# Optimization experiments

Hardware: AMD Instinct MI355X
Metric: run time of the kernel (lower is better)

Reference implementation:

```python
import jax, jax.numpy as jnp
import numpy as np

T, B, I, H = 1024, 64, 512, 512


def setup_inputs() -> dict:
    key = jax.random.key(0)
    ks = jax.random.split(key, 16)
    s = 0.05  # weight init scale
    inp = {
        "x": jax.random.normal(ks[0], (T, B, I), jnp.float32),
        "h0": jax.random.normal(ks[1], (B, H), jnp.float32),
        "c0": jax.random.normal(ks[2], (B, H), jnp.float32),
        "W_ih0f": jax.random.normal(ks[3], (4 * H, I), jnp.float32) * s,
        "W_hh0f": jax.random.normal(ks[4], (4 * H, H), jnp.float32) * s,
        "b0f": jax.random.normal(ks[5], (4 * H,), jnp.float32) * s,
        "W_ih0b": jax.random.normal(ks[6], (4 * H, I), jnp.float32) * s,
        "W_hh0b": jax.random.normal(ks[7], (4 * H, H), jnp.float32) * s,
        "b0b": jax.random.normal(ks[8], (4 * H,), jnp.float32) * s,
        "W_ih1f": jax.random.normal(ks[9], (4 * H, 2 * H), jnp.float32) * s,
        "W_hh1f": jax.random.normal(ks[10], (4 * H, H), jnp.float32) * s,
        "b1f": jax.random.normal(ks[11], (4 * H,), jnp.float32) * s,
        "W_ih1b": jax.random.normal(ks[12], (4 * H, 2 * H), jnp.float32) * s,
        "W_hh1b": jax.random.normal(ks[13], (4 * H, H), jnp.float32) * s,
        "b1b": jax.random.normal(ks[14], (4 * H,), jnp.float32) * s,
    }
    return inp


def _lstm_dir(x, h0, c0, W_ih, W_hh, b, reverse):
    # x: [T, B, in]; precompute input contribution once (big GEMM)
    xg = jnp.einsum('tbi,gi->tbg', x, W_ih) + b  # [T, B, 4H]

    def step(carry, xt):
        h, c = carry
        g = xt + h @ W_hh.T  # [B, 4H]
        i, f, gg, o = jnp.split(g, 4, axis=-1)  # PyTorch LSTMCell gate order
        i = jax.nn.sigmoid(i)
        f = jax.nn.sigmoid(f)
        gg = jnp.tanh(gg)
        o = jax.nn.sigmoid(o)
        c2 = f * c + i * gg
        h2 = o * jnp.tanh(c2)
        return (h2, c2), h2

    (hT, cT), out = jax.lax.scan(step, (h0, c0), xg, reverse=reverse)
    return out, hT, cT  # out[t] aligned with input time t


def reference(x, h0, c0,
              W_ih0f, W_hh0f, b0f, W_ih0b, W_hh0b, b0b,
              W_ih1f, W_hh1f, b1f, W_ih1b, W_hh1b, b1b):
    layers = [
        ((W_ih0f, W_hh0f, b0f), (W_ih0b, W_hh0b, b0b)),
        ((W_ih1f, W_hh1f, b1f), (W_ih1b, W_hh1b, b1b)),
    ]
    inputs = x
    hn, cn = [], []
    for (fw, bw) in layers:
        # NOTE: original reuses the same init_hidden for every layer/direction
        out_f, hf, cf = _lstm_dir(inputs, h0, c0, *fw, reverse=False)
        out_b, hb, cb = _lstm_dir(inputs, h0, c0, *bw, reverse=True)
        hn.append(jnp.concatenate([hf, hb], axis=1))
        cn.append(jnp.concatenate([cf, cb], axis=1))
        inputs = jnp.concatenate([out_f, out_b], axis=2)  # [T, B, 2H]
    hn = jnp.stack(hn, axis=0)  # [L, B, 2H]
    cn = jnp.stack(cn, axis=0)
    return inputs, hn, cn
```

## Files before the change

kernel.cpp:

```cpp
#include <hip/hip_runtime.h>


using bfrag = __attribute__((ext_vector_type(8))) short;
using facc  = __attribute__((ext_vector_type(4))) float;

#define TT 1024
#define NB 64

#define FENCE_PRE(v)  asm volatile("s_nop 3" : "+v"(v))
#define FENCE_POST(v) asm volatile("s_nop 7\n\ts_nop 7" : "+v"(v))

__device__ __forceinline__ unsigned short f2bf(float f) {
  union { float f; unsigned u; } v; v.f = f;
  unsigned r = v.u + 0x7fffu + ((v.u >> 16) & 1u);
  return (unsigned short)(r >> 16);
}
__device__ __forceinline__ float sigm(float x)  { return 1.f / (1.f + __expf(-x)); }
__device__ __forceinline__ float tanhf_(float x){ return 1.f - 2.f / (__expf(2.f * x) + 1.f); }

__device__ __forceinline__ facc mfma_bf16(bfrag a, bfrag b, facc c) {
  asm("v_mfma_f32_16x16x32_bf16 %0, %1, %2, %0" : "+v"(c) : "v"(a), "v"(b));
  return c;
}

__global__ __launch_bounds__(256) void k_cvt_x(const float* __restrict__ x,
                                               unsigned short* __restrict__ xb) {
  int i = blockIdx.x * 256 + threadIdx.x;
  float4 v = reinterpret_cast<const float4*>(x)[i];
  ushort4 o;
  o.x = f2bf(v.x); o.y = f2bf(v.y); o.z = f2bf(v.z); o.w = f2bf(v.w);
  reinterpret_cast<ushort4*>(xb)[i] = o;
}

__global__ __launch_bounds__(256) void k_init(const float* __restrict__ h0,
                                              const float* __restrict__ c0,
                                              unsigned short* __restrict__ h0b,
                                              float* __restrict__ C4) {
  int i = blockIdx.x * 256 + threadIdx.x;
  h0b[i] = f2bf(h0[i]);
  float c = c0[i];
  C4[i] = c; C4[32768 + i] = c; C4[65536 + i] = c; C4[98304 + i] = c;
}

template <int KX>
__global__ __launch_bounds__(256) void k_pack(const float* __restrict__ Wih,
                                              const float* __restrict__ Whh,
                                              const float* __restrict__ bias,
                                              unsigned short* __restrict__ PW,
                                              float* __restrict__ PB) {
  constexpr int K = KX + 512;
  int tid = blockIdx.x * 256 + threadIdx.x;
  int R = tid / K;
  int k = tid - R * K;
  int g = R >> 4, r = R & 15;
  int q = r >> 2, gate = r & 3;
  int srow = gate * 512 + (g * 4 + q);
  float v = (k < KX) ? Wih[srow * KX + k] : Whh[srow * 512 + (k - KX)];
  PW[tid] = f2bf(v);
  if (k == 0) PB[R] = bias[srow];
}

template <int LAYER>
__global__ __launch_bounds__(256) void k_step(
    int s,
    const unsigned short* __restrict__ xin,
    unsigned short* __restrict__ y0,
    float* __restrict__ dout,
    const unsigned short* __restrict__ h0b,
    float* __restrict__ C4,
    unsigned short* __restrict__ hb,
    const unsigned short* __restrict__ PWf, const unsigned short* __restrict__ PWb,
    const float* __restrict__ PBf, const float* __restrict__ PBb) {
  constexpr int KX = (LAYER == 0) ? 512 : 1024;
  constexpr int K  = KX + 512;

  const int bid  = blockIdx.x;
  const int dir  = bid >> 7;
  const int hg   = bid & 127;
  const int t    = dir ? (TT - 1 - s) : s;
  const int wave = threadIdx.x >> 6;
  const int lane = threadIdx.x & 63;
  const int lr   = lane & 15;
  const int lq   = lane >> 4;
  const int b    = wave * 16 + lr;
  const bool first = (s == 0);
  const int tprev  = dir ? (t + 1) : (t - 1);

  const unsigned short* pw = dir ? PWb : PWf;
  const float* pb          = dir ? PBb : PBf;
  const unsigned short* Abase = pw + (size_t)(hg * 16 + lr) * K + lq * 8;

  const unsigned short* xrow = xin + ((size_t)t * NB + b) * (size_t)KX + lq * 8;

  const unsigned short* hrow;
  if (first)            hrow = h0b + (size_t)b * 512 + lq * 8;
  else if (LAYER == 0)  hrow = y0 + ((size_t)tprev * NB + b) * 1024 + dir * 512 + lq * 8;
  else                  hrow = hb + (size_t)((((s & 1) ^ 1) * 2 + dir)) * 32768 + (size_t)b * 512 + lq * 8;

  facc acc = {0.f, 0.f, 0.f, 0.f};
  FENCE_PRE(acc);

#pragma unroll 8
  for (int kk = 0; kk < KX / 32; ++kk) {
    bfrag a = *reinterpret_cast<const bfrag*>(Abase + kk * 32);
    bfrag x = *reinterpret_cast<const bfrag*>(xrow + kk * 32);
    acc = mfma_bf16(a, x, acc);
  }
#pragma unroll 8
  for (int kk = 0; kk < 16; ++kk) {
    bfrag a = *reinterpret_cast<const bfrag*>(Abase + KX + kk * 32);
    bfrag h = *reinterpret_cast<const bfrag*>(hrow + kk * 32);
    acc = mfma_bf16(a, h, acc);
  }
  FENCE_POST(acc);

  const int hcol = hg * 4 + lq;
  const int scan = LAYER * 2 + dir;
  float4 bias = *reinterpret_cast<const float4*>(pb + hg * 16 + lq * 4);
  float ig = sigm(acc[0] + bias.x);
  float fg = sigm(acc[1] + bias.y);
  float gv = tanhf_(acc[2] + bias.z);
  float og = sigm(acc[3] + bias.w);
  const int cidx = scan * 32768 + b * 512 + hcol;
  float c2 = fg * C4[cidx] + ig * gv;
  float h2 = og * tanhf_(c2);
  C4[cidx] = c2;

  const size_t orow = ((size_t)t * NB + b) * 1024 + dir * 512 + hcol;
  if (LAYER == 0) {
    y0[orow] = f2bf(h2);
  } else {
    dout[orow] = h2;
    hb[(size_t)((s & 1) * 2 + dir) * 32768 + (size_t)b * 512 + hcol] = f2bf(h2);
  }

  if (s == TT - 1) {
    const size_t oh = ((size_t)LAYER * NB + b) * 1024 + dir * 512 + hcol;
    dout[67108864 + oh] = h2;
    dout[67239936 + oh] = c2;
  }
}

extern "C" void kernel_launch(void* const* d_in, const int* in_sizes, int n_in,
                              void* d_out, int out_size, void* d_ws, size_t ws_size,
                              hipStream_t stream) {
  (void)in_sizes; (void)n_in; (void)out_size; (void)ws_size;
  const float* x  = (const float*)d_in[0];
  const float* h0 = (const float*)d_in[1];
  const float* c0 = (const float*)d_in[2];
  const float* W[12];
  for (int i = 0; i < 12; ++i) W[i] = (const float*)d_in[3 + i];

  char* ws = (char*)d_ws;
  unsigned short* xb   = (unsigned short*)(ws + 0ull);
  unsigned short* y0   = (unsigned short*)(ws + 67108864ull);
  unsigned short* h0b  = (unsigned short*)(ws + 201326592ull);
  unsigned short* PW0F = (unsigned short*)(ws + 201392128ull);
  unsigned short* PW0B = (unsigned short*)(ws + 205586432ull);
  unsigned short* PW1F = (unsigned short*)(ws + 209780736ull);
  unsigned short* PW1B = (unsigned short*)(ws + 216072192ull);
  float*          PB   = (float*)(ws + 222363648ull);
  float*          C4   = (float*)(ws + 222396416ull);
  unsigned short* hb   = (unsigned short*)(ws + 222920704ull);
  float* dout = (float*)d_out;

  k_cvt_x<<<32768, 256, 0, stream>>>(x, xb);
  k_init<<<128, 256, 0, stream>>>(h0, c0, h0b, C4);
  k_pack<512> <<<8192, 256, 0, stream>>>(W[0], W[1],  W[2],  PW0F, PB + 0);
  k_pack<512> <<<8192, 256, 0, stream>>>(W[3], W[4],  W[5],  PW0B, PB + 2048);
  k_pack<1024><<<12288, 256, 0, stream>>>(W[6], W[7],  W[8],  PW1F, PB + 4096);
  k_pack<1024><<<12288, 256, 0, stream>>>(W[9], W[10], W[11], PW1B, PB + 6144);

  for (int s = 0; s < TT; ++s)
    k_step<0><<<256, 256, 0, stream>>>(s, xb, y0, dout, h0b, C4, hb, PW0F, PW0B, PB + 0,    PB + 2048);
  for (int s = 0; s < TT; ++s)
    k_step<1><<<256, 256, 0, stream>>>(s, y0, y0, dout, h0b, C4, hb, PW1F, PW1B, PB + 4096, PB + 6144);
}
```

Measured before the change: 25.58 ms.

## Split LSTM into chunked input GEMM and persistent cooperative recurrent scan

Replaces the per-timestep kernel launches with two phases per 64-step chunk. First, a batched kernel precomputes the input-gate projection plus bias into a bf16 buffer. Then a persistent cooperative kernel keeps the recurrent weights in registers, stages h in LDS, and syncs its 16 blocks across timesteps with atomic flag polling. This removes about 2048 launch overheads and repeated weight reloads. In exchange, 16 blocks use very little of the GPU, inter-block spin-waits sit on the critical path, and rounding the precomputed gates to bf16 adds error.

Measured after the change: 38.15 ms. 1.49x slower.

```diff
diff --git a/kernel.cpp b/kernel.cpp
--- a/kernel.cpp
+++ b/kernel.cpp
@@ -3,24 +3,38 @@
 
 using bfrag = __attribute__((ext_vector_type(8))) short;
 using facc  = __attribute__((ext_vector_type(4))) float;
-
-#define TT 1024
-#define NB 64
-
-#define FENCE_PRE(v)  asm volatile("s_nop 3" : "+v"(v))
-#define FENCE_POST(v) asm volatile("s_nop 7\n\ts_nop 7" : "+v"(v))
+typedef unsigned long long u64;
 
 __device__ __forceinline__ unsigned short f2bf(float f) {
   union { float f; unsigned u; } v; v.f = f;
   unsigned r = v.u + 0x7fffu + ((v.u >> 16) & 1u);
   return (unsigned short)(r >> 16);
 }
+__device__ __forceinline__ float bf2f(unsigned short u) {
+  union { unsigned u; float f; } v; v.u = ((unsigned)u) << 16; return v.f;
+}
 __device__ __forceinline__ float sigm(float x)  { return 1.f / (1.f + __expf(-x)); }
 __device__ __forceinline__ float tanhf_(float x){ return 1.f - 2.f / (__expf(2.f * x) + 1.f); }
 
 __device__ __forceinline__ facc mfma_bf16(bfrag a, bfrag b, facc c) {
   asm("v_mfma_f32_16x16x32_bf16 %0, %1, %2, %0" : "+v"(c) : "v"(a), "v"(b));
   return c;
+}
+__device__ __forceinline__ u64 pack4bf(facc a) {
+  return (u64)f2bf(a[0]) | ((u64)f2bf(a[1]) << 16)
+       | ((u64)f2bf(a[2]) << 32) | ((u64)f2bf(a[3]) << 48);
+}
+__device__ __forceinline__ u64 ald(const u64* p) {
+  return __hip_atomic_load(p, __ATOMIC_RELAXED, __HIP_MEMORY_SCOPE_AGENT);
+}
+__device__ __forceinline__ unsigned ald32(const unsigned* p) {
+  return __hip_atomic_load(p, __ATOMIC_RELAXED, __HIP_MEMORY_SCOPE_AGENT);
+}
+__device__ __forceinline__ void ast16(unsigned short* p, unsigned short v) {
+  __hip_atomic_store(p, v, __ATOMIC_RELAXED, __HIP_MEMORY_SCOPE_AGENT);
+}
+__device__ __forceinline__ void ast32(unsigned* p, unsigned v) {
+  __hip_atomic_store(p, v, __ATOMIC_RELAXED, __HIP_MEMORY_SCOPE_AGENT);
 }
 
 __global__ __launch_bounds__(256) void k_cvt_x(const float* __restrict__ x,
@@ -35,11 +49,13 @@
 __global__ __launch_bounds__(256) void k_init(const float* __restrict__ h0,
                                               const float* __restrict__ c0,
                                               unsigned short* __restrict__ h0b,
-                                              float* __restrict__ C4) {
+                                              float* __restrict__ cbuf,
+                                              unsigned* __restrict__ hxf) {
   int i = blockIdx.x * 256 + threadIdx.x;
   h0b[i] = f2bf(h0[i]);
   float c = c0[i];
-  C4[i] = c; C4[32768 + i] = c; C4[65536 + i] = c; C4[98304 + i] = c;
+  cbuf[i] = c; cbuf[32768 + i] = c; cbuf[65536 + i] = c; cbuf[98304 + i] = c;
+  if (i < 128) hxf[i] = 0;
 }
 
 template <int KX>
@@ -61,84 +77,180 @@
 }
 
 template <int LAYER>
-__global__ __launch_bounds__(256) void k_step(
-    int s,
+__global__ __launch_bounds__(256) void k_xg(
+    int ph,
     const unsigned short* __restrict__ xin,
-    unsigned short* __restrict__ y0,
-    float* __restrict__ dout,
-    const unsigned short* __restrict__ h0b,
-    float* __restrict__ C4,
-    unsigned short* __restrict__ hb,
+    unsigned short* __restrict__ xgq,
     const unsigned short* __restrict__ PWf, const unsigned short* __restrict__ PWb,
     const float* __restrict__ PBf, const float* __restrict__ PBb) {
   constexpr int KX = (LAYER == 0) ? 512 : 1024;
   constexpr int K  = KX + 512;
-
-  const int bid  = blockIdx.x;
-  const int dir  = bid >> 7;
-  const int hg   = bid & 127;
-  const int t    = dir ? (TT - 1 - s) : s;
-  const int wave = threadIdx.x >> 6;
-  const int lane = threadIdx.x & 63;
-  const int lr   = lane & 15;
-  const int lq   = lane >> 4;
-  const int b    = wave * 16 + lr;
-  const bool first = (s == 0);
-  const int tprev  = dir ? (t + 1) : (t - 1);
-
+  const int bid = blockIdx.x;
+  const int dir = bid >> 7, hg = bid & 127;
+  const int wv = threadIdx.x >> 6, lane = threadIdx.x & 63;
+  const int lr = lane & 15, lq = lane >> 4;
+  const int b = wv * 16 + lr;
   const unsigned short* pw = dir ? PWb : PWf;
   const float* pb          = dir ? PBb : PBf;
   const unsigned short* Abase = pw + (size_t)(hg * 16 + lr) * K + lq * 8;
-
-  const unsigned short* xrow = xin + ((size_t)t * NB + b) * (size_t)KX + lq * 8;
-
-  const unsigned short* hrow;
-  if (first)            hrow = h0b + (size_t)b * 512 + lq * 8;
-  else if (LAYER == 0)  hrow = y0 + ((size_t)tprev * NB + b) * 1024 + dir * 512 + lq * 8;
-  else                  hrow = hb + (size_t)((((s & 1) ^ 1) * 2 + dir)) * 32768 + (size_t)b * 512 + lq * 8;
-
-  facc acc = {0.f, 0.f, 0.f, 0.f};
-  FENCE_PRE(acc);
-
+  const float4 bias = *reinterpret_cast<const float4*>(pb + hg * 16 + lq * 4);
+
+  for (int sl = 0; sl < 64; ++sl) {
+    const int s = ph * 64 + sl;
+    const int t = dir ? (1023 - s) : s;
+    const unsigned short* xrow = xin + ((size_t)t * 64 + b) * KX + lq * 8;
+    facc acc = {0.f, 0.f, 0.f, 0.f};
+    asm volatile("s_nop 3" : "+v"(acc));
 #pragma unroll 8
-  for (int kk = 0; kk < KX / 32; ++kk) {
-    bfrag a = *reinterpret_cast<const bfrag*>(Abase + kk * 32);
-    bfrag x = *reinterpret_cast<const bfrag*>(xrow + kk * 32);
-    acc = mfma_bf16(a, x, acc);
+    for (int kk = 0; kk < KX / 32; ++kk) {
+      bfrag a  = *reinterpret_cast<const bfrag*>(Abase + kk * 32);
+      bfrag xf = *reinterpret_cast<const bfrag*>(xrow + kk * 32);
+      acc = mfma_bf16(a, xf, acc);
+    }
+    asm volatile("s_nop 7\n\ts_nop 7" : "+v"(acc));
+    acc[0] += bias.x; acc[1] += bias.y; acc[2] += bias.z; acc[3] += bias.w;
+    u64* dst = reinterpret_cast<u64*>(
+        xgq + (((size_t)dir * 64 + sl) * 64 + b) * 2048 + hg * 16 + lq * 4);
+    *dst = pack4bf(acc);
   }
-#pragma unroll 8
-  for (int kk = 0; kk < 16; ++kk) {
-    bfrag a = *reinterpret_cast<const bfrag*>(Abase + KX + kk * 32);
-    bfrag h = *reinterpret_cast<const bfrag*>(hrow + kk * 32);
-    acc = mfma_bf16(a, h, acc);
+}
+
+template <int LAYER>
+__global__ __launch_bounds__(512, 2) void k_scan(
+    int ph,
+    const unsigned short* __restrict__ xgq,
+    unsigned short* __restrict__ y0,
+    float* __restrict__ dout,
+    const unsigned short* __restrict__ h0b,
+    float* __restrict__ cbuf,
+    unsigned short* __restrict__ hx,
+    const unsigned short* __restrict__ PWf, const unsigned short* __restrict__ PWb,
+    unsigned* __restrict__ hxf) {
+  constexpr int KX = (LAYER == 0) ? 512 : 1024;
+  constexpr int K  = KX + 512;
+  extern __shared__ unsigned short Hlds[];
+
+  const int bid = blockIdx.x;
+  const int dir = bid & 1, g = bid >> 1;
+  const int tid = threadIdx.x;
+  const int w = tid >> 6, lane = tid & 63;
+  const int lr = lane & 15, lq = lane >> 4;
+  const unsigned short* pw = dir ? PWb : PWf;
+  unsigned* hxfd = hxf + (LAYER * 2 + dir) * 16;
+
+  bfrag Wreg[32];
+#pragma unroll
+  for (int rtl = 0; rtl < 2; ++rtl)
+#pragma unroll
+    for (int kt = 0; kt < 16; ++kt)
+      Wreg[rtl * 16 + kt] = *reinterpret_cast<const bfrag*>(
+          pw + (size_t)((g * 16 + w * 2 + rtl) * 16 + lr) * K + KX + kt * 32 + lq * 8);
+
+  const int slot = LAYER * 2 + dir;
+  float cst[2][4];
+#pragma unroll
+  for (int rtl = 0; rtl < 2; ++rtl)
+#pragma unroll
+    for (int bt = 0; bt < 4; ++bt)
+      cst[rtl][bt] = cbuf[((size_t)slot * 64 + bt * 16 + lr) * 512
+                          + g * 64 + w * 8 + rtl * 4 + lq];
+
+  for (int sl = 0; sl < 64; ++sl) {
+    const int s = ph * 64 + sl;
+    const int t = dir ? (1023 - s) : s;
+
+    u64 xv[2][4];
+#pragma unroll
+    for (int rtl = 0; rtl < 2; ++rtl)
+#pragma unroll
+      for (int bt = 0; bt < 4; ++bt)
+        xv[rtl][bt] = *reinterpret_cast<const u64*>(
+            xgq + (((size_t)dir * 64 + sl) * 64 + bt * 16 + lr) * 2048
+                + g * 256 + w * 32 + rtl * 16 + lq * 4);
+
+    if (s > 0) {
+      while (ald32(&hxfd[lane & 7]) < (unsigned)s) __builtin_amdgcn_s_sleep(8);
+    }
+    __syncthreads();
+
+    const unsigned short* hsrc = (s == 0)
+        ? h0b : hx + (size_t)(dir * 2 + ((s - 1) & 1)) * 32768;
+#pragma unroll
+    for (int it = 0; it < 8; ++it) {
+      const int sidx = it * 512 + tid;
+      const int C = sidx >> 4, lrs = sidx & 15;
+      const int kts = C >> 4, bts = (C >> 2) & 3, lqs = C & 3;
+      const int src = (bts * 16 + lrs) * 512 + kts * 32 + lqs * 8;
+      u64 d0 = ald(reinterpret_cast<const u64*>(hsrc + src));
+      u64 d1 = ald(reinterpret_cast<const u64*>(hsrc + src + 4));
+      u64* dp = reinterpret_cast<u64*>(Hlds + sidx * 8);
+      dp[0] = d0; dp[1] = d1;
+    }
+    __syncthreads();
+
+    facc acc[2][4];
+#pragma unroll
+    for (int rtl = 0; rtl < 2; ++rtl)
+#pragma unroll
+      for (int bt = 0; bt < 4; ++bt) {
+        acc[rtl][bt][0] = bf2f((unsigned short)(xv[rtl][bt] & 0xffff));
+        acc[rtl][bt][1] = bf2f((unsigned short)((xv[rtl][bt] >> 16) & 0xffff));
+        acc[rtl][bt][2] = bf2f((unsigned short)((xv[rtl][bt] >> 32) & 0xffff));
+        acc[rtl][bt][3] = bf2f((unsigned short)((xv[rtl][bt] >> 48) & 0xffff));
+      }
+    asm volatile("s_nop 3"
+                 : "+v"(acc[0][0]), "+v"(acc[0][1]), "+v"(acc[0][2]), "+v"(acc[0][3]),
+                   "+v"(acc[1][0]), "+v"(acc[1][1]), "+v"(acc[1][2]), "+v"(acc[1][3]));
+#pragma unroll
+    for (int kt = 0; kt < 16; ++kt) {
+      bfrag Bv[4];
+#pragma unroll
+      for (int bt = 0; bt < 4; ++bt)
+        Bv[bt] = *reinterpret_cast<const bfrag*>(
+            Hlds + (((kt * 4 + bt) * 4 + lq) * 16 + lr) * 8);
+#pragma unroll
+      for (int rtl = 0; rtl < 2; ++rtl)
+#pragma unroll
+        for (int bt = 0; bt < 4; ++bt)
+          acc[rtl][bt] = mfma_bf16(Wreg[rtl * 16 + kt], Bv[bt], acc[rtl][bt]);
+    }
+    asm volatile("s_nop 7\n\ts_nop 7"
+                 : "+v"(acc[0][0]), "+v"(acc[0][1]), "+v"(acc[0][2]), "+v"(acc[0][3]),
+                   "+v"(acc[1][0]), "+v"(acc[1][1]), "+v"(acc[1][2]), "+v"(acc[1][3]));
+
+#pragma unroll
+    for (int rtl = 0; rtl < 2; ++rtl)
+#pragma unroll
+      for (int bt = 0; bt < 4; ++bt) {
+        float ig = sigm(acc[rtl][bt][0]);
+        float fg = sigm(acc[rtl][bt][1]);
+        float gv = tanhf_(acc[rtl][bt][2]);
+        float og = sigm(acc[rtl][bt][3]);
+        cst[rtl][bt] = fg * cst[rtl][bt] + ig * gv;
+        const float h2 = og * tanhf_(cst[rtl][bt]);
+        const int b = bt * 16 + lr;
+        const int hcol = g * 64 + w * 8 + rtl * 4 + lq;
+        ast16(&hx[(size_t)(dir * 2 + (s & 1)) * 32768 + (size_t)b * 512 + hcol],
+              f2bf(h2));
+        const size_t orow = ((size_t)t * 64 + b) * 1024 + dir * 512 + hcol;
+        if constexpr (LAYER == 0) y0[orow] = f2bf(h2);
+        else                      dout[orow] = h2;
+        if (s == 1023) {
+          const size_t oh = ((size_t)LAYER * 64 + b) * 1024 + dir * 512 + hcol;
+          dout[67108864 + oh] = h2;
+          dout[67239936 + oh] = cst[rtl][bt];
+        }
+      }
+    __syncthreads();
+    if (tid == 0) ast32(&hxfd[g], (unsigned)(s + 1));
   }
-  FENCE_POST(acc);
-
-  const int hcol = hg * 4 + lq;
-  const int scan = LAYER * 2 + dir;
-  float4 bias = *reinterpret_cast<const float4*>(pb + hg * 16 + lq * 4);
-  float ig = sigm(acc[0] + bias.x);
-  float fg = sigm(acc[1] + bias.y);
-  float gv = tanhf_(acc[2] + bias.z);
-  float og = sigm(acc[3] + bias.w);
-  const int cidx = scan * 32768 + b * 512 + hcol;
-  float c2 = fg * C4[cidx] + ig * gv;
-  float h2 = og * tanhf_(c2);
-  C4[cidx] = c2;
-
-  const size_t orow = ((size_t)t * NB + b) * 1024 + dir * 512 + hcol;
-  if (LAYER == 0) {
-    y0[orow] = f2bf(h2);
-  } else {
-    dout[orow] = h2;
-    hb[(size_t)((s & 1) * 2 + dir) * 32768 + (size_t)b * 512 + hcol] = f2bf(h2);
-  }
-
-  if (s == TT - 1) {
-    const size_t oh = ((size_t)LAYER * NB + b) * 1024 + dir * 512 + hcol;
-    dout[67108864 + oh] = h2;
-    dout[67239936 + oh] = c2;
-  }
+
+#pragma unroll
+  for (int rtl = 0; rtl < 2; ++rtl)
+#pragma unroll
+    for (int bt = 0; bt < 4; ++bt)
+      cbuf[((size_t)slot * 64 + bt * 16 + lr) * 512
+           + g * 64 + w * 8 + rtl * 4 + lq] = cst[rtl][bt];
 }
 
 extern "C" void kernel_launch(void* const* d_in, const int* in_sizes, int n_in,
@@ -154,25 +266,52 @@
   char* ws = (char*)d_ws;
   unsigned short* xb   = (unsigned short*)(ws + 0ull);
   unsigned short* y0   = (unsigned short*)(ws + 67108864ull);
-  unsigned short* h0b  = (unsigned short*)(ws + 201326592ull);
-  unsigned short* PW0F = (unsigned short*)(ws + 201392128ull);
-  unsigned short* PW0B = (unsigned short*)(ws + 205586432ull);
-  unsigned short* PW1F = (unsigned short*)(ws + 209780736ull);
-  unsigned short* PW1B = (unsigned short*)(ws + 216072192ull);
-  float*          PB   = (float*)(ws + 222363648ull);
-  float*          C4   = (float*)(ws + 222396416ull);
-  unsigned short* hb   = (unsigned short*)(ws + 222920704ull);
+  unsigned short* xgq  = (unsigned short*)(ws + 201326592ull);
+  unsigned short* PW0F = (unsigned short*)(ws + 234881024ull);
+  unsigned short* PW0B = (unsigned short*)(ws + 239075328ull);
+  unsigned short* PW1F = (unsigned short*)(ws + 243269632ull);
+  unsigned short* PW1B = (unsigned short*)(ws + 249561088ull);
+  float*          PB   = (float*)(ws + 255852544ull);
+  unsigned short* h0b  = (unsigned short*)(ws + 255885312ull);
+  float*          cbuf = (float*)(ws + 255950848ull);
+  unsigned short* hx   = (unsigned short*)(ws + 256475136ull);
+  unsigned*       hxf  = (unsigned*)(ws + 256737280ull);
   float* dout = (float*)d_out;
 
   k_cvt_x<<<32768, 256, 0, stream>>>(x, xb);
-  k_init<<<128, 256, 0, stream>>>(h0, c0, h0b, C4);
+  k_init<<<128, 256, 0, stream>>>(h0, c0, h0b, cbuf, hxf);
   k_pack<512> <<<8192, 256, 0, stream>>>(W[0], W[1],  W[2],  PW0F, PB + 0);
   k_pack<512> <<<8192, 256, 0, stream>>>(W[3], W[4],  W[5],  PW0B, PB + 2048);
   k_pack<1024><<<12288, 256, 0, stream>>>(W[6], W[7],  W[8],  PW1F, PB + 4096);
   k_pack<1024><<<12288, 256, 0, stream>>>(W[9], W[10], W[11], PW1B, PB + 6144);
 
-  for (int s = 0; s < TT; ++s)
-    k_step<0><<<256, 256, 0, stream>>>(s, xb, y0, dout, h0b, C4, hb, PW0F, PW0B, PB + 0,    PB + 2048);
-  for (int s = 0; s < TT; ++s)
-    k_step<1><<<256, 256, 0, stream>>>(s, y0, y0, dout, h0b, C4, hb, PW1F, PW1B, PB + 4096, PB + 6144);
-}
+  (void)hipFuncSetAttribute((const void*)(&k_scan<0>),
+                            hipFuncAttributeMaxDynamicSharedMemorySize, 65536);
+  (void)hipFuncSetAttribute((const void*)(&k_scan<1>),
+                            hipFuncAttributeMaxDynamicSharedMemorySize, 65536);
+
+  unsigned short *xgqp = xgq, *y0p = y0, *h0bp = h0b, *hxp = hx;
+  float *cbufp = cbuf;
+  unsigned* hxfp = hxf;
+  const unsigned short *pw0f = PW0F, *pw0b = PW0B, *pw1f = PW1F, *pw1b = PW1B;
+  float* doutp = dout;
+
+  for (int ph = 0; ph < 16; ++ph) {
+    k_xg<0><<<256, 256, 0, stream>>>(ph, xb, xgq, PW0F, PW0B, PB + 0, PB + 2048);
+    int phv = ph;
+    void* as[] = {(void*)&phv, (void*)&xgqp, (void*)&y0p, (void*)&doutp,
+                  (void*)&h0bp, (void*)&cbufp, (void*)&hxp,
+                  (void*)&pw0f, (void*)&pw0b, (void*)&hxfp};
+    (void)hipLaunchCooperativeKernel((const void*)(&k_scan<0>), dim3(16), dim3(512),
+                                     as, 65536, stream);
+  }
+  for (int ph = 0; ph < 16; ++ph) {
+    k_xg<1><<<256, 256, 0, stream>>>(ph, y0, xgq, PW1F, PW1B, PB + 4096, PB + 6144);
+    int phv = ph;
+    void* as[] = {(void*)&phv, (void*)&xgqp, (void*)&y0p, (void*)&doutp,
+                  (void*)&h0bp, (void*)&cbufp, (void*)&hxp,
+                  (void*)&pw1f, (void*)&pw1b, (void*)&hxfp};
+    (void)hipLaunchCooperativeKernel((const void*)(&k_scan<1>), dim3(16), dim3(512),
+                                     as, 65536, stream);
+  }
+}
```
